# Kernel optimization log

Measured on AMD Instinct MI355X. Metric: run time of the kernel, lower is better.

## Reference

```python
import jax, jax.numpy as jnp
import numpy as np

KEY_DIM = 32
VALUE_DIM = 64
HEADS = 8
CHAN = 256


def conv1x1(x, w, b):
    # x: [b, c, h, w], w: [out, c], b: [out]  (1x1 conv == channel matmul)
    return jnp.einsum('bchw,oc->bohw', x, w) + b[None, :, None, None]


def setup_inputs() -> dict:
    key = jax.random.key(0)
    ks = jax.random.split(key, 9)
    b, c, h, w = 8, CHAN, 128, 128
    qk_dim = KEY_DIM * HEADS   # 256
    v_dim = VALUE_DIM * HEADS  # 512
    s = 0.02
    return {
        'x':  jax.random.normal(ks[0], (b, c, h, w), jnp.float32),
        'Wq': jax.random.normal(ks[1], (qk_dim, c), jnp.float32) * s,
        'bq': jnp.zeros((qk_dim,), jnp.float32),
        'Wk': jax.random.normal(ks[2], (qk_dim, c), jnp.float32) * s,
        'bk': jnp.zeros((qk_dim,), jnp.float32),
        'Wv': jax.random.normal(ks[3], (v_dim, c), jnp.float32) * s,
        'bv': jnp.zeros((v_dim,), jnp.float32),
        'Wo': jax.random.normal(ks[4], (c, v_dim), jnp.float32) * s,
        'bo': jnp.zeros((c,), jnp.float32),
    }


def reference(x, Wq, bq, Wk, bk, Wv, bv, Wo, bo):
    b, c, h, w = x.shape
    n = h * w
    scale = KEY_DIM ** (-0.25)
    # 1x1 conv projections, reshape to [b, heads, d, n]
    q = conv1x1(x, Wq, bq).reshape(b, HEADS, KEY_DIM, n) * scale
    k = conv1x1(x, Wk, bk).reshape(b, HEADS, KEY_DIM, n) * scale
    v = conv1x1(x, Wv, bv).reshape(b, HEADS, VALUE_DIM, n)
    # softmax over sequence positions for keys
    k = jax.nn.softmax(k, axis=-1)
    # norm_queries=True: softmax over key dim for queries
    q = jax.nn.softmax(q, axis=-2)
    # linear attention: context [b,h,d_k,d_v], then output [b,h,d_v,n]
    ctx = jnp.einsum('bhdn,bhen->bhde', k, v)
    out = jnp.einsum('bhdn,bhde->bhen', q, ctx)
    out = out.reshape(b, HEADS * VALUE_DIM, h, w)
    return conv1x1(out, Wo, bo)
```

## Files before the change

### kernel.cpp

```cpp
#include <hip/hip_runtime.h>
#include <hip/hip_bf16.h>
#include <cstddef>


constexpr int   NPIX     = 16384;
constexpr float QK_SCALE = 0.42044820762685725f;
constexpr int   NCH      = 16;

typedef __attribute__((ext_vector_type(8))) short          bf16x8;
typedef __attribute__((ext_vector_type(8))) unsigned short u16x8;
typedef __attribute__((ext_vector_type(4))) float          f32x4;

__device__ __forceinline__ float bf2f(unsigned short v) {
    union { unsigned int u; float f; } c; c.u = ((unsigned int)v) << 16; return c.f;
}
__device__ __forceinline__ unsigned short f2bf(float f) {
    union { __hip_bfloat16 h; unsigned short s; } c; c.h = __float2bfloat16(f); return c.s;
}
__device__ __forceinline__ void gload_lds16(const void* g, void* l) {
    __builtin_amdgcn_global_load_lds(
        (const __attribute__((address_space(1))) unsigned int*)g,
        (__attribute__((address_space(3))) unsigned int*)l, 16, 0, 0);
}

typedef unsigned short lds_row32[32];

__global__ __launch_bounds__(256) void prep(
    const float* __restrict__ Wq, const float* __restrict__ Wk,
    unsigned short* __restrict__ Wqb, unsigned short* __restrict__ Wkb)
{
    const int i = blockIdx.x * 256 + threadIdx.x;
    Wqb[i] = f2bf(Wq[i]);
    Wkb[i] = f2bf(Wk[i]);
}

template<bool QPASS>
__global__ __launch_bounds__(256, 3) void proj_mfma(
    const float* __restrict__ x, const unsigned short* __restrict__ Wb,
    const float* __restrict__ bias, unsigned short* __restrict__ eout,
    float* __restrict__ ksump2)
{
    __shared__ alignas(16) unsigned char smem[18432];
    lds_row32* As1 = (lds_row32*)smem;
    unsigned short (*BsT)[40] = (unsigned short(*)[40])(smem + 8192);
    const int b  = blockIdx.z;
    const int m0 = blockIdx.y * 128;
    const int n0 = blockIdx.x * 128;
    const int t  = threadIdx.x;
    const int w  = t >> 6, l = t & 63;
    const int lm = l & 15, lg = l >> 4;
    const int mwl = (w & 1) * 64;
    const int nwl = (w >> 1) * 64;
    const int lgs = (lg ^ ((lm & 3) ^ ((lm >> 2) & 3))) * 8;
    const int r16 = l >> 2;
    const int scb = ((l & 3) ^ ((r16 & 3) ^ ((r16 >> 2) & 3))) * 8;

    const unsigned short* Abase = Wb + (size_t)m0 * 256;
    const float* xb = x + (size_t)b * 256 * NPIX + n0;
    const int np = (t & 63) * 2, kq = (t >> 6) * 8;

    f32x4 acc[4][4] = {};
    for (int k0 = 0; k0 < 256; k0 += 32) {
        #pragma unroll
        for (int i = 0; i < 2; ++i) {
            const int row0 = w*32 + i*16;
            gload_lds16(Abase + (size_t)(row0 + r16)*256 + k0 + scb, &As1[row0][0]);
        }
        {
            const float* src = xb + (size_t)(k0 + kq) * NPIX + np;
            float2 v[8];
            #pragma unroll
            for (int r = 0; r < 8; ++r)
                v[r] = *(const float2*)(src + (size_t)r * NPIX);
            u16x8 pa, pb;
            #pragma unroll
            for (int r = 0; r < 8; ++r) { pa[r] = f2bf(v[r].x); pb[r] = f2bf(v[r].y); }
            *(u16x8*)&BsT[np][kq]     = pa;
            *(u16x8*)&BsT[np + 1][kq] = pb;
        }
        __syncthreads();
        bf16x8 afr[4], bfr[4];
        #pragma unroll
        for (int i = 0; i < 4; ++i)
            afr[i] = *(const bf16x8*)&As1[mwl + i*16 + lm][lgs];
        #pragma unroll
        for (int j = 0; j < 4; ++j)
            bfr[j] = *(const bf16x8*)&BsT[nwl + j*16 + lm][lg*8];
        #pragma unroll
        for (int i = 0; i < 4; ++i)
            #pragma unroll
            for (int j = 0; j < 4; ++j)
                acc[i][j] = __builtin_amdgcn_mfma_f32_16x16x32_bf16(afr[i], bfr[j], acc[i][j], 0, 0, 0);
        __syncthreads();
    }

    unsigned short (*Cs)[64][72] = (unsigned short(*)[64][72])smem;
    const int mw = m0 + mwl, nw = n0 + nwl;
    const int cw = w & 1;
    const int ph = w >> 1;

    #pragma unroll
    for (int phase = 0; phase < 2; ++phase) {
        if (ph == phase) {
            float ksloc[4][4];
            #pragma unroll
            for (int i = 0; i < 4; ++i) {
                const f32x4 bb4 = *(const f32x4*)(bias + mw + i*16 + lg*4);
                #pragma unroll
                for (int r = 0; r < 4; ++r) {
                    const int row = i*16 + lg*4 + r;
                    float cs = 0.f;
                    #pragma unroll
                    for (int j = 0; j < 4; ++j) {
                        const int col = j*16 + lm;
                        const unsigned short bs = f2bf(__expf(QK_SCALE * (acc[i][j][r] + bb4[r])));
                        if (QPASS) Cs[cw][col][row] = bs;
                        else { Cs[cw][row][col] = bs; cs += bf2f(bs); }
                    }
                    ksloc[i][r] = cs;
                }
            }
            if (!QPASS) {
                #pragma unroll
                for (int i = 0; i < 4; ++i)
                    #pragma unroll
                    for (int r = 0; r < 4; ++r) {
                        float v = ksloc[i][r];
                        v += __shfl_xor(v, 1, 64);
                        v += __shfl_xor(v, 2, 64);
                        v += __shfl_xor(v, 4, 64);
                        v += __shfl_xor(v, 8, 64);
                        if (lm == 0) {
                            const int nt2 = blockIdx.x * 2 + (w >> 1);
                            ksump2[((size_t)b*256 + nt2)*256 + mw + i*16 + lg*4 + r] = v;
                        }
                    }
            }
        }
        __syncthreads();
        if (ph == phase) {
            if (QPASS) {
                unsigned short* dst = eout + ((size_t)b * NPIX + nw + l) * 256 + mw;
                u16x8 vv[8];
                float z0 = 0.f, z1 = 0.f;
                #pragma unroll
                for (int s8 = 0; s8 < 8; ++s8) {
                    vv[s8] = *(const u16x8*)&Cs[cw][l][s8*8];
                    float ps = 0.f;
                    #pragma unroll
                    for (int u = 0; u < 8; ++u) ps += bf2f(vv[s8][u]);
                    if (s8 < 4) z0 += ps; else z1 += ps;
                }
                const float iz0 = 1.0f / z0, iz1 = 1.0f / z1;
                #pragma unroll
                for (int s8 = 0; s8 < 8; ++s8) {
                    const float iz = (s8 < 4) ? iz0 : iz1;
                    u16x8 o;
                    #pragma unroll
                    for (int u = 0; u < 8; ++u) o[u] = f2bf(bf2f(vv[s8][u]) * iz);
                    *(u16x8*)(dst + s8*8) = o;
                }
            } else {
                unsigned short* dst = eout + ((size_t)b * 256 + mw + l) * NPIX + nw;
                #pragma unroll
                for (int s8 = 0; s8 < 8; ++s8)
                    *(u16x8*)(dst + s8*8) = *(const u16x8*)&Cs[cw][l][s8*8];
            }
        }
        __syncthreads();
    }
}

__global__ __launch_bounds__(256) void ksum_red(
    const float* __restrict__ ksump2, float* __restrict__ ksum)
{
    const int t = threadIdx.x;
    const int row = blockIdx.x * 32 + (t >> 3);
    const int b = row >> 8, c = row & 255;
    const int nt0 = t & 7;
    float s = 0.f;
    #pragma unroll 8
    for (int i = 0; i < 32; ++i)
        s += ksump2[((size_t)b*256 + nt0 + 8*i)*256 + c];
    s += __shfl_xor(s, 1, 64);
    s += __shfl_xor(s, 2, 64);
    s += __shfl_xor(s, 4, 64);
    if (nt0 == 0) ksum[row] = s;
}

__global__ __launch_bounds__(256) void t_mfma(
    const unsigned short* __restrict__ ek, const float* __restrict__ x,
    float* __restrict__ Tpart)
{
    __shared__ alignas(16) unsigned char smem[32768];
    lds_row32* As = (lds_row32*)smem;
    lds_row32* Bs = (lds_row32*)(smem + 16384);
    const int bid  = blockIdx.x;
    const int v    = bid & 7, s = bid >> 3;
    const int gidx = s >> 2, q = s & 3;
    const int group = v + 8 * gidx;
    const int b = group / NCH, chunk = group % NCH;
    const int mt = (q >> 1) * 128, ct = (q & 1) * 128;
    constexpr int CHPX = NPIX / NCH;

    const int t = threadIdx.x;
    const int w = t >> 6, l = t & 63;
    const int lm = l & 15, lg = l >> 4;
    const int mw = (w & 1) * 64, cw = (w >> 1) * 64;
    const int r16 = l >> 2;
    const int scb = ((l & 3) ^ ((r16 & 3) ^ ((r16 >> 2) & 3))) * 8;
    const int lgs = (lg ^ ((lm & 3) ^ ((lm >> 2) & 3))) * 8;
    const int brq = t >> 3;
    const int bc4 = (t & 7) * 4;
    const int bslot = (t & 7) >> 1;
    const int bhalf = (t & 1) * 4;

    const unsigned short* Abase = ek + ((size_t)b*256 + mt) * NPIX;
    const float*          Bbase = x  + ((size_t)b*256 + ct) * NPIX;
    const int p0base = chunk * CHPX;

    f32x4 breg[4];
    f32x4 acc[4][4] = {};

    #pragma unroll
    for (int i = 0; i < 2; ++i) {
        const int row0 = w*32 + i*16;
        gload_lds16(Abase + (size_t)(row0 + r16) * NPIX + p0base + scb, &As[row0][0]);
    }
    #pragma unroll
    for (int it = 0; it < 4; ++it)
        breg[it] = *(const f32x4*)(Bbase + (size_t)(it*32 + brq) * NPIX + p0base + bc4);
    #pragma unroll
    for (int it = 0; it < 4; ++it) {
        const int row = it*32 + brq;
        const int sl = bslot ^ ((row & 3) ^ ((row >> 2) & 3));
        unsigned short o[4] = { f2bf(breg[it].x), f2bf(breg[it].y),
                                f2bf(breg[it].z), f2bf(breg[it].w) };
        *(ushort4*)&Bs[row][sl*8 + bhalf] = *(ushort4*)o;
    }
    __syncthreads();

    constexpr int ITERS = CHPX / 32;
    for (int t8 = 0; t8 < ITERS; ++t8) {
        const int cur = t8 & 1;
        if (t8 < ITERS - 1) {
            const int p0 = p0base + (t8 + 1) * 32;
            #pragma unroll
            for (int i = 0; i < 2; ++i) {
                const int row0 = w*32 + i*16;
                gload_lds16(Abase + (size_t)(row0 + r16) * NPIX + p0 + scb,
                            &As[(cur^1)*128 + row0][0]);
            }
            #pragma unroll
            for (int it = 0; it < 4; ++it)
                breg[it] = *(const f32x4*)(Bbase + (size_t)(it*32 + brq) * NPIX + p0 + bc4);
        }
        bf16x8 afr[4], bfr[4];
        #pragma unroll
        for (int i = 0; i < 4; ++i)
            afr[i] = *(const bf16x8*)&As[cur*128 + mw + i*16 + lm][lgs];
        #pragma unroll
        for (int j = 0; j < 4; ++j)
            bfr[j] = *(const bf16x8*)&Bs[cur*128 + cw + j*16 + lm][lgs];
        #pragma unroll
        for (int i = 0; i < 4; ++i)
            #pragma unroll
            for (int j = 0; j < 4; ++j)
                acc[i][j] = __builtin_amdgcn_mfma_f32_16x16x32_bf16(afr[i], bfr[j], acc[i][j], 0, 0, 0);
        if (t8 < ITERS - 1) {
            #pragma unroll
            for (int it = 0; it < 4; ++it) {
                const int row = it*32 + brq;
                const int sl = bslot ^ ((row & 3) ^ ((row >> 2) & 3));
                unsigned short o[4] = { f2bf(breg[it].x), f2bf(breg[it].y),
                                        f2bf(breg[it].z), f2bf(breg[it].w) };
                *(ushort4*)&Bs[(cur^1)*128 + row][sl*8 + bhalf] = *(ushort4*)o;
            }
        }
        __syncthreads();
    }

    float* dst = Tpart + ((size_t)(b*NCH + chunk) * 256) * 256;
    #pragma unroll
    for (int i = 0; i < 4; ++i)
        #pragma unroll
        for (int r = 0; r < 4; ++r) {
            const int gm = mt + mw + i*16 + lg*4 + r;
            #pragma unroll
            for (int j = 0; j < 4; ++j)
                dst[(size_t)gm * 256 + ct + cw + j*16 + lm] = acc[i][j][r];
        }
}

__global__ __launch_bounds__(256) void treduce(
    float* __restrict__ Tpart, const float* __restrict__ ksum)
{
    const int gid = blockIdx.x * 256 + threadIdx.x;
    const int b   = gid >> 14;
    const int rem = gid & 16383;
    const int r   = rem >> 6;
    const int c4  = (rem & 63) * 4;
    float* base = Tpart + (((size_t)b*NCH) * 256 + r) * 256 + c4;
    f32x4 s = *(f32x4*)base;
    #pragma unroll
    for (int ch = 1; ch < NCH; ++ch) {
        f32x4 v = *(const f32x4*)(base + (size_t)ch * 65536);
        s.x += v.x; s.y += v.y; s.z += v.z; s.w += v.w;
    }
    const float inv = 1.0f / ksum[b*256 + r];
    s.x *= inv; s.y *= inv; s.z *= inv; s.w *= inv;
    *(f32x4*)base = s;
}

__global__ __launch_bounds__(256) void ctx_pass(
    const float* __restrict__ Tpart, const float* __restrict__ Wv,
    const float* __restrict__ bv, float* __restrict__ ctx)
{
    const int gid = blockIdx.x * 256 + threadIdx.x;
    const int b   = gid >> 14;
    const int rem = gid & 16383;
    const int h   = rem >> 11;
    const int de  = rem & 2047;
    const int d   = de >> 6;
    const int e   = de & 63;
    const float* tp = Tpart + (((size_t)b*NCH) * 256 + h*32 + d) * 256;
    const float* wv = Wv + (size_t)(h*64 + e) * 256;
    float sx = 0.f, sy = 0.f, sz = 0.f, sw = 0.f;
    #pragma unroll 8
    for (int c = 0; c < 256; c += 4) {
        f32x4 a = *(const f32x4*)(tp + c);
        f32x4 wv4 = *(const f32x4*)(wv + c);
        sx = fmaf(a.x, wv4.x, sx); sy = fmaf(a.y, wv4.y, sy);
        sz = fmaf(a.z, wv4.z, sz); sw = fmaf(a.w, wv4.w, sw);
    }
    ctx[gid] = (sx + sy) + (sz + sw) + bv[h*64 + e];
}

__global__ __launch_bounds__(256) void mpass(
    const float* __restrict__ ctx, const float* __restrict__ Wo,
    unsigned short* __restrict__ Mb)
{
    const int gid = blockIdx.x * 256 + threadIdx.x;
    const int b   = gid >> 16;
    const int rem = gid & 65535;
    const int o   = rem >> 8;
    const int dg  = rem & 255;
    const int h   = dg >> 5;
    const float* cp = ctx + ((size_t)b*8 + h) * 2048 + (dg & 31) * 64;
    const float* wp = Wo + (size_t)o * 512 + h*64;
    float sx = 0.f, sy = 0.f, sz = 0.f, sw = 0.f;
    #pragma unroll
    for (int e = 0; e < 64; e += 4) {
        f32x4 a = *(const f32x4*)(cp + e);
        f32x4 wv = *(const f32x4*)(wp + e);
        sx = fmaf(a.x, wv.x, sx); sy = fmaf(a.y, wv.y, sy);
        sz = fmaf(a.z, wv.z, sz); sw = fmaf(a.w, wv.w, sw);
    }
    Mb[((size_t)b*256 + o) * 256 + dg] = f2bf((sx + sy) + (sz + sw));
}

__global__ __launch_bounds__(256) void out_mfma(
    const unsigned short* __restrict__ eqT, const unsigned short* __restrict__ Mb,
    const float* __restrict__ bo, float* __restrict__ out)
{
    __shared__ alignas(16) unsigned char smem[32768];
    lds_row32* As0 = (lds_row32*)smem;
    lds_row32* Bs0 = (lds_row32*)(smem + 16384);
    const int b  = blockIdx.z;
    const int m0 = blockIdx.y * 128;
    const int n0 = blockIdx.x * 128;
    const int t  = threadIdx.x;
    const int w  = t >> 6, l = t & 63;
    const int lm = l & 15, lg = l >> 4;
    const int mwl = (w & 1) * 64, nwl = (w >> 1) * 64;
    const int lgs = (lg ^ ((lm & 3) ^ ((lm >> 2) & 3))) * 8;
    const int r16 = l >> 2;
    const int scb = ((l & 3) ^ ((r16 & 3) ^ ((r16 >> 2) & 3))) * 8;

    const unsigned short* Abase = Mb  + ((size_t)b*256 + m0) * 256;
    const unsigned short* Bbase = eqT + ((size_t)b*NPIX + n0) * 256;

    auto stage = [&](int buf, int k0) {
        #pragma unroll
        for (int i = 0; i < 2; ++i) {
            const int row0 = w*32 + i*16;
            gload_lds16(Abase + (size_t)(row0 + r16)*256 + k0 + scb, &As0[buf*128 + row0][0]);
            gload_lds16(Bbase + (size_t)(row0 + r16)*256 + k0 + scb, &Bs0[buf*128 + row0][0]);
        }
    };

    f32x4 acc[4][4] = {};
    stage(0, 0);
    __syncthreads();
    for (int t8 = 0; t8 < 8; ++t8) {
        const int cur = t8 & 1;
        if (t8 < 7) stage(cur ^ 1, (t8 + 1) * 32);
        bf16x8 afr[4], bfr[4];
        #pragma unroll
        for (int i = 0; i < 4; ++i)
            afr[i] = *(const bf16x8*)&As0[cur*128 + mwl + i*16 + lm][lgs];
        #pragma unroll
        for (int j = 0; j < 4; ++j)
            bfr[j] = *(const bf16x8*)&Bs0[cur*128 + nwl + j*16 + lm][lgs];
        #pragma unroll
        for (int i = 0; i < 4; ++i)
            #pragma unroll
            for (int j = 0; j < 4; ++j)
                acc[i][j] = __builtin_amdgcn_mfma_f32_16x16x32_bf16(afr[i], bfr[j], acc[i][j], 0, 0, 0);
        __syncthreads();
    }

    #pragma unroll
    for (int i = 0; i < 4; ++i) {
        const f32x4 bb4 = *(const f32x4*)(bo + m0 + mwl + i*16 + lg*4);
        #pragma unroll
        for (int r = 0; r < 4; ++r) {
            const int gm = m0 + mwl + i*16 + lg*4 + r;
            float* dst = out + ((size_t)b*256 + gm) * NPIX + n0 + nwl;
            #pragma unroll
            for (int j = 0; j < 4; ++j)
                dst[j*16 + lm] = acc[i][j][r] + bb4[r];
        }
    }
}

extern "C" void kernel_launch(void* const* d_in, const int* in_sizes, int n_in,
                              void* d_out, int out_size, void* d_ws, size_t ws_size,
                              hipStream_t stream)
{
    const float* x  = (const float*)d_in[0];
    const float* Wq = (const float*)d_in[1];
    const float* bq = (const float*)d_in[2];
    const float* Wk = (const float*)d_in[3];
    const float* bk = (const float*)d_in[4];
    const float* Wv = (const float*)d_in[5];
    const float* bv = (const float*)d_in[6];
    const float* Wo = (const float*)d_in[7];
    const float* bo = (const float*)d_in[8];
    float* out = (float*)d_out;
    char* wsb = (char*)d_ws;

    if (ws_size < (size_t)102506496) return;

    unsigned short* ekq   = (unsigned short*)wsb;
    float*          Tpart = (float*)(wsb + 67108864);
    float*          ksump2= (float*)(wsb + 67108864);
    float*          ctx   = (float*)(wsb + 100663296);
    float*          ksum  = (float*)(wsb + 101187584);
    unsigned short* Mb    = (unsigned short*)(wsb + 101195776);
    unsigned short* Wqb   = (unsigned short*)(wsb + 102244352);
    unsigned short* Wkb   = (unsigned short*)(wsb + 102375424);

    prep            <<<256,             256, 0, stream>>>(Wq, Wk, Wqb, Wkb);
    proj_mfma<false><<<dim3(128, 2, 8), 256, 0, stream>>>(x, Wkb, bk, ekq, ksump2);
    ksum_red        <<<64,              256, 0, stream>>>(ksump2, ksum);
    t_mfma          <<<512,             256, 0, stream>>>(ekq, x, Tpart);
    treduce         <<<512,             256, 0, stream>>>(Tpart, ksum);
    ctx_pass        <<<512,             256, 0, stream>>>(Tpart, Wv, bv, ctx);
    mpass           <<<2048,            256, 0, stream>>>(ctx, Wo, Mb);
    proj_mfma<true> <<<dim3(128, 2, 8), 256, 0, stream>>>(x, Wqb, bq, ekq, ksump2);
    out_mfma        <<<dim3(128, 2, 8), 256, 0, stream>>>(ekq, Mb, bo, out);
}
```

Measured before the change: 261.0 us.

## Cache transposed bf16 x in K projection and reuse it for Q projection

The K-projection kernel now also writes a pixel-major bf16 copy of x, from the m0==0 blocks only. The Q-projection kernel is rewritten to read that copy with direct global-to-LDS loads and double buffering, instead of re-reading fp32 x and converting it. The epilogues are simplified to use all four waves at once rather than two phases, which doubles LDS use per block and drops the occupancy hint. The extra 64MB write and larger workspace are traded against halving Q-pass input traffic and removing the per-tile conversion.

```diff
diff --git a/kernel.cpp b/kernel.cpp
--- a/kernel.cpp
+++ b/kernel.cpp
@@ -34,15 +34,14 @@
     Wkb[i] = f2bf(Wk[i]);
 }
 
-template<bool QPASS>
-__global__ __launch_bounds__(256, 3) void proj_mfma(
+__global__ __launch_bounds__(256) void proj_k(
     const float* __restrict__ x, const unsigned short* __restrict__ Wb,
     const float* __restrict__ bias, unsigned short* __restrict__ eout,
-    float* __restrict__ ksump2)
-{
-    __shared__ alignas(16) unsigned char smem[18432];
+    unsigned short* __restrict__ xTb, float* __restrict__ ksump2)
+{
+    __shared__ alignas(16) unsigned char smem[36864];
     lds_row32* As1 = (lds_row32*)smem;
-    unsigned short (*BsT)[40] = (unsigned short(*)[40])(smem + 8192);
+    unsigned short (*BsT)[40] = (unsigned short(*)[40])(smem + 16384);
     const int b  = blockIdx.z;
     const int m0 = blockIdx.y * 128;
     const int n0 = blockIdx.x * 128;
@@ -77,6 +76,11 @@
             for (int r = 0; r < 8; ++r) { pa[r] = f2bf(v[r].x); pb[r] = f2bf(v[r].y); }
             *(u16x8*)&BsT[np][kq]     = pa;
             *(u16x8*)&BsT[np + 1][kq] = pb;
+            if (m0 == 0) {
+                unsigned short* xd = xTb + ((size_t)b*NPIX + n0 + np) * 256 + k0 + kq;
+                *(u16x8*)xd         = pa;
+                *(u16x8*)(xd + 256) = pb;
+            }
         }
         __syncthreads();
         bf16x8 afr[4], bfr[4];
@@ -96,78 +100,131 @@
 
     unsigned short (*Cs)[64][72] = (unsigned short(*)[64][72])smem;
     const int mw = m0 + mwl, nw = n0 + nwl;
-    const int cw = w & 1;
-    const int ph = w >> 1;
-
-    #pragma unroll
-    for (int phase = 0; phase < 2; ++phase) {
-        if (ph == phase) {
-            float ksloc[4][4];
-            #pragma unroll
-            for (int i = 0; i < 4; ++i) {
-                const f32x4 bb4 = *(const f32x4*)(bias + mw + i*16 + lg*4);
-                #pragma unroll
-                for (int r = 0; r < 4; ++r) {
-                    const int row = i*16 + lg*4 + r;
-                    float cs = 0.f;
-                    #pragma unroll
-                    for (int j = 0; j < 4; ++j) {
-                        const int col = j*16 + lm;
-                        const unsigned short bs = f2bf(__expf(QK_SCALE * (acc[i][j][r] + bb4[r])));
-                        if (QPASS) Cs[cw][col][row] = bs;
-                        else { Cs[cw][row][col] = bs; cs += bf2f(bs); }
-                    }
-                    ksloc[i][r] = cs;
-                }
+    float ksloc[4][4];
+    #pragma unroll
+    for (int i = 0; i < 4; ++i) {
+        const f32x4 bb4 = *(const f32x4*)(bias + mw + i*16 + lg*4);
+        #pragma unroll
+        for (int r = 0; r < 4; ++r) {
+            const int row = i*16 + lg*4 + r;
+            float cs = 0.f;
+            #pragma unroll
+            for (int j = 0; j < 4; ++j) {
+                const int col = j*16 + lm;
+                const unsigned short bs = f2bf(__expf(QK_SCALE * (acc[i][j][r] + bb4[r])));
+                Cs[w][row][col] = bs;
+                cs += bf2f(bs);
             }
-            if (!QPASS) {
-                #pragma unroll
-                for (int i = 0; i < 4; ++i)
-                    #pragma unroll
-                    for (int r = 0; r < 4; ++r) {
-                        float v = ksloc[i][r];
-                        v += __shfl_xor(v, 1, 64);
-                        v += __shfl_xor(v, 2, 64);
-                        v += __shfl_xor(v, 4, 64);
-                        v += __shfl_xor(v, 8, 64);
-                        if (lm == 0) {
-                            const int nt2 = blockIdx.x * 2 + (w >> 1);
-                            ksump2[((size_t)b*256 + nt2)*256 + mw + i*16 + lg*4 + r] = v;
-                        }
-                    }
+            ksloc[i][r] = cs;
+        }
+    }
+    #pragma unroll
+    for (int i = 0; i < 4; ++i)
+        #pragma unroll
+        for (int r = 0; r < 4; ++r) {
+            float v = ksloc[i][r];
+            v += __shfl_xor(v, 1, 64);
+            v += __shfl_xor(v, 2, 64);
+            v += __shfl_xor(v, 4, 64);
+            v += __shfl_xor(v, 8, 64);
+            if (lm == 0) {
+                const int nt2 = blockIdx.x * 2 + (w >> 1);
+                ksump2[((size_t)b*256 + nt2)*256 + mw + i*16 + lg*4 + r] = v;
             }
         }
+    __syncthreads();
+    unsigned short* dst = eout + ((size_t)b * 256 + mw + l) * NPIX + nw;
+    #pragma unroll
+    for (int s8 = 0; s8 < 8; ++s8)
+        *(u16x8*)(dst + s8*8) = *(const u16x8*)&Cs[w][l][s8*8];
+}
+
+__global__ __launch_bounds__(256) void proj_q_xt(
+    const unsigned short* __restrict__ xTb, const unsigned short* __restrict__ Wb,
+    const float* __restrict__ bias, unsigned short* __restrict__ eout)
+{
+    __shared__ alignas(16) unsigned char smem[36864];
+    lds_row32* As = (lds_row32*)smem;
+    lds_row32* Bs = (lds_row32*)(smem + 16384);
+    const int b  = blockIdx.z;
+    const int m0 = blockIdx.y * 128;
+    const int n0 = blockIdx.x * 128;
+    const int t  = threadIdx.x;
+    const int w  = t >> 6, l = t & 63;
+    const int lm = l & 15, lg = l >> 4;
+    const int mwl = (w & 1) * 64, nwl = (w >> 1) * 64;
+    const int lgs = (lg ^ ((lm & 3) ^ ((lm >> 2) & 3))) * 8;
+    const int r16 = l >> 2;
+    const int scb = ((l & 3) ^ ((r16 & 3) ^ ((r16 >> 2) & 3))) * 8;
+
+    const unsigned short* Abase = Wb + (size_t)m0 * 256;
+    const unsigned short* Bbase = xTb + ((size_t)b*NPIX + n0) * 256;
+
+    auto stage = [&](int buf, int k0) {
+        #pragma unroll
+        for (int i = 0; i < 2; ++i) {
+            const int row0 = w*32 + i*16;
+            gload_lds16(Abase + (size_t)(row0 + r16)*256 + k0 + scb, &As[buf*128 + row0][0]);
+            gload_lds16(Bbase + (size_t)(row0 + r16)*256 + k0 + scb, &Bs[buf*128 + row0][0]);
+        }
+    };
+
+    f32x4 acc[4][4] = {};
+    stage(0, 0);
+    __syncthreads();
+    for (int t8 = 0; t8 < 8; ++t8) {
+        const int cur = t8 & 1;
+        if (t8 < 7) stage(cur ^ 1, (t8 + 1) * 32);
+        bf16x8 afr[4], bfr[4];
+        #pragma unroll
+        for (int i = 0; i < 4; ++i)
+            afr[i] = *(const bf16x8*)&As[cur*128 + mwl + i*16 + lm][lgs];
+        #pragma unroll
+        for (int j = 0; j < 4; ++j)
+            bfr[j] = *(const bf16x8*)&Bs[cur*128 + nwl + j*16 + lm][lgs];
+        #pragma unroll
+        for (int i = 0; i < 4; ++i)
+            #pragma unroll
+            for (int j = 0; j < 4; ++j)
+                acc[i][j] = __builtin_amdgcn_mfma_f32_16x16x32_bf16(afr[i], bfr[j], acc[i][j], 0, 0, 0);
         __syncthreads();
-        if (ph == phase) {
-            if (QPASS) {
-                unsigned short* dst = eout + ((size_t)b * NPIX + nw + l) * 256 + mw;
-                u16x8 vv[8];
-                float z0 = 0.f, z1 = 0.f;
-                #pragma unroll
-                for (int s8 = 0; s8 < 8; ++s8) {
-                    vv[s8] = *(const u16x8*)&Cs[cw][l][s8*8];
-                    float ps = 0.f;
-                    #pragma unroll
-                    for (int u = 0; u < 8; ++u) ps += bf2f(vv[s8][u]);
-                    if (s8 < 4) z0 += ps; else z1 += ps;
-                }
-                const float iz0 = 1.0f / z0, iz1 = 1.0f / z1;
-                #pragma unroll
-                for (int s8 = 0; s8 < 8; ++s8) {
-                    const float iz = (s8 < 4) ? iz0 : iz1;
-                    u16x8 o;
-                    #pragma unroll
-                    for (int u = 0; u < 8; ++u) o[u] = f2bf(bf2f(vv[s8][u]) * iz);
-                    *(u16x8*)(dst + s8*8) = o;
-                }
-            } else {
-                unsigned short* dst = eout + ((size_t)b * 256 + mw + l) * NPIX + nw;
-                #pragma unroll
-                for (int s8 = 0; s8 < 8; ++s8)
-                    *(u16x8*)(dst + s8*8) = *(const u16x8*)&Cs[cw][l][s8*8];
+    }
+
+    unsigned short (*Cs)[64][72] = (unsigned short(*)[64][72])smem;
+    const int mw = m0 + mwl, nw = n0 + nwl;
+    #pragma unroll
+    for (int i = 0; i < 4; ++i) {
+        const f32x4 bb4 = *(const f32x4*)(bias + mw + i*16 + lg*4);
+        #pragma unroll
+        for (int r = 0; r < 4; ++r) {
+            const int row = i*16 + lg*4 + r;
+            #pragma unroll
+            for (int j = 0; j < 4; ++j) {
+                const int col = j*16 + lm;
+                Cs[w][col][row] = f2bf(__expf(QK_SCALE * (acc[i][j][r] + bb4[r])));
             }
         }
-        __syncthreads();
+    }
+    __syncthreads();
+    unsigned short* dst = eout + ((size_t)b * NPIX + nw + l) * 256 + mw;
+    u16x8 vv[8];
+    float z0 = 0.f, z1 = 0.f;
+    #pragma unroll
+    for (int s8 = 0; s8 < 8; ++s8) {
+        vv[s8] = *(const u16x8*)&Cs[w][l][s8*8];
+        float ps = 0.f;
+        #pragma unroll
+        for (int u = 0; u < 8; ++u) ps += bf2f(vv[s8][u]);
+        if (s8 < 4) z0 += ps; else z1 += ps;
+    }
+    const float iz0 = 1.0f / z0, iz1 = 1.0f / z1;
+    #pragma unroll
+    for (int s8 = 0; s8 < 8; ++s8) {
+        const float iz = (s8 < 4) ? iz0 : iz1;
+        u16x8 o;
+        #pragma unroll
+        for (int u = 0; u < 8; ++u) o[u] = f2bf(bf2f(vv[s8][u]) * iz);
+        *(u16x8*)(dst + s8*8) = o;
     }
 }
 
@@ -440,7 +497,7 @@
     float* out = (float*)d_out;
     char* wsb = (char*)d_ws;
 
-    if (ws_size < (size_t)102506496) return;
+    if (ws_size < (size_t)169615360) return;
 
     unsigned short* ekq   = (unsigned short*)wsb;
     float*          Tpart = (float*)(wsb + 67108864);
@@ -450,14 +507,15 @@
     unsigned short* Mb    = (unsigned short*)(wsb + 101195776);
     unsigned short* Wqb   = (unsigned short*)(wsb + 102244352);
     unsigned short* Wkb   = (unsigned short*)(wsb + 102375424);
-
-    prep            <<<256,             256, 0, stream>>>(Wq, Wk, Wqb, Wkb);
-    proj_mfma<false><<<dim3(128, 2, 8), 256, 0, stream>>>(x, Wkb, bk, ekq, ksump2);
-    ksum_red        <<<64,              256, 0, stream>>>(ksump2, ksum);
-    t_mfma          <<<512,             256, 0, stream>>>(ekq, x, Tpart);
-    treduce         <<<512,             256, 0, stream>>>(Tpart, ksum);
-    ctx_pass        <<<512,             256, 0, stream>>>(Tpart, Wv, bv, ctx);
-    mpass           <<<2048,            256, 0, stream>>>(ctx, Wo, Mb);
-    proj_mfma<true> <<<dim3(128, 2, 8), 256, 0, stream>>>(x, Wqb, bq, ekq, ksump2);
-    out_mfma        <<<dim3(128, 2, 8), 256, 0, stream>>>(ekq, Mb, bo, out);
-}
+    unsigned short* xTb   = (unsigned short*)(wsb + 102506496);
+
+    prep     <<<256,             256, 0, stream>>>(Wq, Wk, Wqb, Wkb);
+    proj_k   <<<dim3(128, 2, 8), 256, 0, stream>>>(x, Wkb, bk, ekq, xTb, ksump2);
+    ksum_red <<<64,              256, 0, stream>>>(ksump2, ksum);
+    t_mfma   <<<512,             256, 0, stream>>>(ekq, x, Tpart);
+    treduce  <<<512,             256, 0, stream>>>(Tpart, ksum);
+    ctx_pass <<<512,             256, 0, stream>>>(Tpart, Wv, bv, ctx);
+    mpass    <<<2048,            256, 0, stream>>>(ctx, Wo, Mb);
+    proj_q_xt<<<dim3(128, 2, 8), 256, 0, stream>>>(xTb, Wqb, bq, ekq);
+    out_mfma <<<dim3(128, 2, 8), 256, 0, stream>>>(ekq, Mb, bo, out);
+}
```

Measured after the change: 295.8 us. +13.4%, slower.
